# Kernel tuning notes

Measured on AMD Instinct MI355X. Metric: run time of the kernel, lower is better.

## Reference

```python
import jax, jax.numpy as jnp
import numpy as np

B, C, H, W = 64, 1, 1024, 1024
NEG_WEIGHT = 0.1  # constant loss contribution where target != 1


def setup_inputs() -> dict:
    key = jax.random.key(0)
    k1, k2 = jax.random.split(key)
    prediction = jax.random.normal(k1, (B, C, H, W), dtype=jnp.float32)
    target = jax.random.randint(k2, (B, C, H, W), 0, 2, dtype=jnp.int32)
    return {"prediction": prediction, "target": target}


def reference(prediction, target):
    # loss_i = 1 - sigmoid(pred_i) if target_i == 1 else 0.1; return mean over all elements
    p = jax.nn.sigmoid(prediction)
    loss = jnp.where(target == 1, 1.0 - p, jnp.float32(NEG_WEIGHT))
    return jnp.mean(loss)
```

## Files before the change

### kernel.cpp

```cpp
#include <hip/hip_runtime.h>


#define BLOCK 256
#define GRID  2048

typedef float vf4 __attribute__((ext_vector_type(4)));
typedef int   vi4 __attribute__((ext_vector_type(4)));

__device__ __forceinline__ float loss4(vf4 p, vi4 t) {
    float l0 = (t.x == 1) ? 1.0f / (1.0f + __expf(p.x)) : 0.1f;
    float l1 = (t.y == 1) ? 1.0f / (1.0f + __expf(p.y)) : 0.1f;
    float l2 = (t.z == 1) ? 1.0f / (1.0f + __expf(p.z)) : 0.1f;
    float l3 = (t.w == 1) ? 1.0f / (1.0f + __expf(p.w)) : 0.1f;
    return (l0 + l1) + (l2 + l3);
}

__device__ __forceinline__ void block_reduce_atomic(float acc, float inv_n,
                                                    float* __restrict__ out) {
#pragma unroll
    for (int off = 32; off > 0; off >>= 1)
        acc += __shfl_down(acc, off, 64);
    __shared__ float smem[BLOCK / 64];
    const int lane = threadIdx.x & 63;
    const int wave = threadIdx.x >> 6;
    if (lane == 0) smem[wave] = acc;
    __syncthreads();
    if (threadIdx.x == 0) {
        float bsum = (smem[0] + smem[1]) + (smem[2] + smem[3]);
        atomicAdd(out, bsum * inv_n);
    }
}

__global__ __launch_bounds__(BLOCK)
void wloss_nt(const vf4* __restrict__ p4,
              const vi4* __restrict__ t4,
              float* __restrict__ out,
              int iters, int stride, float inv_n) {
    int i = blockIdx.x * BLOCK + threadIdx.x;

    vf4 pA = __builtin_nontemporal_load(&p4[i]);
    vi4 tA = __builtin_nontemporal_load(&t4[i]);
    vf4 pB = __builtin_nontemporal_load(&p4[i + stride]);
    vi4 tB = __builtin_nontemporal_load(&t4[i + stride]);
    int idx = i + 2 * stride;

    float acc = 0.0f;
    for (int k = 0; k < iters - 2; ++k) {
        vf4 pN = __builtin_nontemporal_load(&p4[idx]);
        vi4 tN = __builtin_nontemporal_load(&t4[idx]);
        idx += stride;
        acc += loss4(pA, tA);
        pA = pB; tA = tB;
        pB = pN; tB = tN;
    }
    acc += loss4(pA, tA);
    acc += loss4(pB, tB);

    block_reduce_atomic(acc, inv_n, out);
}

__global__ __launch_bounds__(BLOCK)
void wloss_generic(const float* __restrict__ pred,
                   const int*   __restrict__ tgt,
                   float* __restrict__ out,
                   long long n, float inv_n) {
    const long long n4     = n >> 2;
    const long long tid    = (long long)blockIdx.x * blockDim.x + threadIdx.x;
    const long long stride = (long long)gridDim.x * blockDim.x;

    const vf4* p4 = (const vf4*)pred;
    const vi4* t4 = (const vi4*)tgt;

    float acc = 0.0f;
    for (long long i = tid; i < n4; i += stride)
        acc += loss4(p4[i], t4[i]);
    if (blockIdx.x == 0) {
        for (long long i = (n4 << 2) + threadIdx.x; i < n; i += blockDim.x)
            acc += (tgt[i] == 1) ? 1.0f / (1.0f + __expf(pred[i])) : 0.1f;
    }
    block_reduce_atomic(acc, inv_n, out);
}

extern "C" void kernel_launch(void* const* d_in, const int* in_sizes, int n_in,
                              void* d_out, int out_size, void* d_ws, size_t ws_size,
                              hipStream_t stream) {
    const float* pred = (const float*)d_in[0];
    const int*   tgt  = (const int*)d_in[1];
    float*       out  = (float*)d_out;

    const long long n = (long long)in_sizes[0];
    const float inv_n = 1.0f / (float)n;

    hipMemsetAsync(out, 0, sizeof(float), stream);

    const long long n4 = n >> 2;
    const long long stride = (long long)GRID * BLOCK;

    if ((n & 3) == 0 && n4 % stride == 0 && n4 / stride >= 2) {
        const int iters = (int)(n4 / stride);
        wloss_nt<<<GRID, BLOCK, 0, stream>>>((const vf4*)pred,
                                             (const vi4*)tgt, out,
                                             iters, (int)stride, inv_n);
    } else {
        long long g = (n4 + BLOCK - 1) / BLOCK;
        if (g > 8192) g = 8192;
        if (g < 1)    g = 1;
        wloss_generic<<<(int)g, BLOCK, 0, stream>>>(pred, tgt, out, n, inv_n);
    }
}
```

Baseline: 482.8 us.

## Split into target bitmask pass and prediction pass using workspace

Splits the fused kernel in two. The first kernel packs the target into a 1-bit-per-element ballot mask in workspace and adds the constant 0.1 contributions. The second kernel reads the predictions plus that small mask to sum the sigmoid terms. The total bytes read from global memory stay about the same, plus an extra mask write and read and a second launch, so there is no clear bandwidth saving for this memory-bound reduction.

New measurement: 521.4 us. 8.0% more time.

```diff
diff --git a/kernel.cpp b/kernel.cpp
--- a/kernel.cpp
+++ b/kernel.cpp
@@ -6,6 +6,8 @@
 
 typedef float vf4 __attribute__((ext_vector_type(4)));
 typedef int   vi4 __attribute__((ext_vector_type(4)));
+typedef unsigned long long u64;
+typedef u64 vu2 __attribute__((ext_vector_type(2)));
 
 __device__ __forceinline__ float loss4(vf4 p, vi4 t) {
     float l0 = (t.x == 1) ? 1.0f / (1.0f + __expf(p.x)) : 0.1f;
@@ -15,7 +17,7 @@
     return (l0 + l1) + (l2 + l3);
 }
 
-__device__ __forceinline__ void block_reduce_atomic(float acc, float inv_n,
+__device__ __forceinline__ void block_reduce_atomic(float acc, float scale,
                                                     float* __restrict__ out) {
 #pragma unroll
     for (int off = 32; off > 0; off >>= 1)
@@ -27,8 +29,89 @@
     __syncthreads();
     if (threadIdx.x == 0) {
         float bsum = (smem[0] + smem[1]) + (smem[2] + smem[3]);
-        atomicAdd(out, bsum * inv_n);
-    }
+        atomicAdd(out, bsum * scale);
+    }
+}
+
+__device__ __forceinline__ void tproc(vi4 t, int chunk, int lane,
+                                      u64* __restrict__ mask, int& cnt0) {
+    u64 b0 = __ballot(t.x == 1);
+    u64 b1 = __ballot(t.y == 1);
+    u64 b2 = __ballot(t.z == 1);
+    u64 b3 = __ballot(t.w == 1);
+    cnt0 += (t.x != 1) + (t.y != 1) + (t.z != 1) + (t.w != 1);
+    if (lane < 4) {
+        u64 b = (lane == 0) ? b0 : (lane == 1) ? b1 : (lane == 2) ? b2 : b3;
+        mask[(size_t)chunk * 4 + lane] = b;
+    }
+}
+
+__global__ __launch_bounds__(BLOCK)
+void tgt_mask(const vi4* __restrict__ t4, u64* __restrict__ mask,
+              float* __restrict__ out, int iters, int stride, float inv_n) {
+    const int tid  = threadIdx.x;
+    const int lane = tid & 63;
+    const int wv   = tid >> 6;
+    const int cstep = stride >> 6;
+
+    int i     = blockIdx.x * BLOCK + tid;
+    int chunk = blockIdx.x * (BLOCK / 64) + wv;
+
+    vi4 tA = __builtin_nontemporal_load(&t4[i]);
+    vi4 tB = __builtin_nontemporal_load(&t4[i + stride]);
+    int idx = i + 2 * stride;
+
+    int cnt0 = 0;
+    for (int k = 0; k < iters - 2; ++k) {
+        vi4 tN = __builtin_nontemporal_load(&t4[idx]);
+        idx += stride;
+        tproc(tA, chunk, lane, mask, cnt0);
+        chunk += cstep;
+        tA = tB; tB = tN;
+    }
+    tproc(tA, chunk, lane, mask, cnt0); chunk += cstep;
+    tproc(tB, chunk, lane, mask, cnt0);
+
+    block_reduce_atomic(0.1f * (float)cnt0, inv_n, out);
+}
+
+__device__ __forceinline__ float pproc(vf4 p, const u64* __restrict__ mp, int lane) {
+    vu2 m01 = *(const vu2*)(mp);
+    vu2 m23 = *(const vu2*)(mp + 2);
+    float l0 = ((m01.x >> lane) & 1ull) ? 1.0f / (1.0f + __expf(p.x)) : 0.0f;
+    float l1 = ((m01.y >> lane) & 1ull) ? 1.0f / (1.0f + __expf(p.y)) : 0.0f;
+    float l2 = ((m23.x >> lane) & 1ull) ? 1.0f / (1.0f + __expf(p.z)) : 0.0f;
+    float l3 = ((m23.y >> lane) & 1ull) ? 1.0f / (1.0f + __expf(p.w)) : 0.0f;
+    return (l0 + l1) + (l2 + l3);
+}
+
+__global__ __launch_bounds__(BLOCK)
+void pred_loss(const vf4* __restrict__ p4, const u64* __restrict__ mask,
+               float* __restrict__ out, int iters, int stride, float inv_n) {
+    const int tid  = threadIdx.x;
+    const int lane = tid & 63;
+    const int wv   = tid >> 6;
+    const int cstep = stride >> 6;
+
+    int i     = blockIdx.x * BLOCK + tid;
+    int chunk = blockIdx.x * (BLOCK / 64) + wv;
+
+    vf4 pA = __builtin_nontemporal_load(&p4[i]);
+    vf4 pB = __builtin_nontemporal_load(&p4[i + stride]);
+    int idx = i + 2 * stride;
+
+    float acc = 0.0f;
+    for (int k = 0; k < iters - 2; ++k) {
+        vf4 pN = __builtin_nontemporal_load(&p4[idx]);
+        idx += stride;
+        acc += pproc(pA, mask + (size_t)chunk * 4, lane);
+        chunk += cstep;
+        pA = pB; pB = pN;
+    }
+    acc += pproc(pA, mask + (size_t)chunk * 4, lane); chunk += cstep;
+    acc += pproc(pB, mask + (size_t)chunk * 4, lane);
+
+    block_reduce_atomic(acc, inv_n, out);
 }
 
 __global__ __launch_bounds__(BLOCK)
@@ -95,8 +178,17 @@
 
     const long long n4 = n >> 2;
     const long long stride = (long long)GRID * BLOCK;
-
-    if ((n & 3) == 0 && n4 % stride == 0 && n4 / stride >= 2) {
+    const bool tiled = ((n & 3) == 0) && (n4 % stride == 0) && (n4 / stride >= 3);
+    const size_t mask_bytes = (size_t)(n >> 3);
+
+    if (tiled && d_ws != nullptr && ws_size >= mask_bytes) {
+        const int iters = (int)(n4 / stride);
+        u64* mask = (u64*)d_ws;
+        tgt_mask <<<GRID, BLOCK, 0, stream>>>((const vi4*)tgt, mask, out,
+                                              iters, (int)stride, inv_n);
+        pred_loss<<<GRID, BLOCK, 0, stream>>>((const vf4*)pred, mask, out,
+                                              iters, (int)stride, inv_n);
+    } else if (tiled) {
         const int iters = (int)(n4 / stride);
         wloss_nt<<<GRID, BLOCK, 0, stream>>>((const vf4*)pred,
                                              (const vi4*)tgt, out,
```

## Stream inputs through LDS with global_load_lds double buffering

Applied to the files above, without the earlier changes.

The main streaming kernel now fetches prediction and target tiles with direct global-to-LDS loads into a two-slot shared buffer, reads them back from LDS and syncs the block each iteration. Register-held prefetch is dropped so more loads can be in flight without using VGPRs. In exchange it adds a block barrier per iteration and an extra LDS read. It also loses the nontemporal hint, and the 16-byte global_load_lds width may not be supported on every target.

After: 507.0 us. 5.0% more time.

```diff
diff --git a/kernel.cpp b/kernel.cpp
--- a/kernel.cpp
+++ b/kernel.cpp
@@ -7,6 +7,9 @@
 typedef float vf4 __attribute__((ext_vector_type(4)));
 typedef int   vi4 __attribute__((ext_vector_type(4)));
 
+typedef const __attribute__((address_space(1))) void glb_v;
+typedef __attribute__((address_space(3))) void lds_v;
+
 __device__ __forceinline__ float loss4(vf4 p, vi4 t) {
     float l0 = (t.x == 1) ? 1.0f / (1.0f + __expf(p.x)) : 0.1f;
     float l1 = (t.y == 1) ? 1.0f / (1.0f + __expf(p.y)) : 0.1f;
@@ -15,7 +18,7 @@
     return (l0 + l1) + (l2 + l3);
 }
 
-__device__ __forceinline__ void block_reduce_atomic(float acc, float inv_n,
+__device__ __forceinline__ void block_reduce_atomic(float acc, float scale,
                                                     float* __restrict__ out) {
 #pragma unroll
     for (int off = 32; off > 0; off >>= 1)
@@ -27,34 +30,41 @@
     __syncthreads();
     if (threadIdx.x == 0) {
         float bsum = (smem[0] + smem[1]) + (smem[2] + smem[3]);
-        atomicAdd(out, bsum * inv_n);
+        atomicAdd(out, bsum * scale);
     }
 }
 
 __global__ __launch_bounds__(BLOCK)
-void wloss_nt(const vf4* __restrict__ p4,
-              const vi4* __restrict__ t4,
-              float* __restrict__ out,
-              int iters, int stride, float inv_n) {
-    int i = blockIdx.x * BLOCK + threadIdx.x;
+void wl_main_dma(const vf4* __restrict__ p4,
+                 const vi4* __restrict__ t4,
+                 float* __restrict__ out,
+                 int iters, int stride, float inv_n) {
+    __shared__ vf4 lp[2][BLOCK];
+    __shared__ vi4 lt[2][BLOCK];
 
-    vf4 pA = __builtin_nontemporal_load(&p4[i]);
-    vi4 tA = __builtin_nontemporal_load(&t4[i]);
-    vf4 pB = __builtin_nontemporal_load(&p4[i + stride]);
-    vi4 tB = __builtin_nontemporal_load(&t4[i + stride]);
-    int idx = i + 2 * stride;
+    const int tid = threadIdx.x;
+    const int wv  = tid >> 6;
+    int idx = blockIdx.x * BLOCK + tid;
+
+    __builtin_amdgcn_global_load_lds((glb_v*)&p4[idx], (lds_v*)&lp[0][wv * 64], 16, 0, 0);
+    __builtin_amdgcn_global_load_lds((glb_v*)&t4[idx], (lds_v*)&lt[0][wv * 64], 16, 0, 0);
+    __syncthreads();
 
     float acc = 0.0f;
-    for (int k = 0; k < iters - 2; ++k) {
-        vf4 pN = __builtin_nontemporal_load(&p4[idx]);
-        vi4 tN = __builtin_nontemporal_load(&t4[idx]);
+    int cur = 0;
+    for (int k = 0; k < iters - 1; ++k) {
         idx += stride;
-        acc += loss4(pA, tA);
-        pA = pB; tA = tB;
-        pB = pN; tB = tN;
+        __builtin_amdgcn_global_load_lds((glb_v*)&p4[idx], (lds_v*)&lp[cur ^ 1][wv * 64], 16, 0, 0);
+        __builtin_amdgcn_global_load_lds((glb_v*)&t4[idx], (lds_v*)&lt[cur ^ 1][wv * 64], 16, 0, 0);
+        vf4 p = lp[cur][tid];
+        vi4 t = lt[cur][tid];
+        acc += loss4(p, t);
+        __syncthreads();
+        cur ^= 1;
     }
-    acc += loss4(pA, tA);
-    acc += loss4(pB, tB);
+    vf4 p = lp[cur][tid];
+    vi4 t = lt[cur][tid];
+    acc += loss4(p, t);
 
     block_reduce_atomic(acc, inv_n, out);
 }
@@ -95,12 +105,13 @@
 
     const long long n4 = n >> 2;
     const long long stride = (long long)GRID * BLOCK;
+    const bool tiled = ((n & 3) == 0) && (n4 % stride == 0) && (n4 / stride >= 2);
 
-    if ((n & 3) == 0 && n4 % stride == 0 && n4 / stride >= 2) {
+    if (tiled) {
         const int iters = (int)(n4 / stride);
-        wloss_nt<<<GRID, BLOCK, 0, stream>>>((const vf4*)pred,
-                                             (const vi4*)tgt, out,
-                                             iters, (int)stride, inv_n);
+        wl_main_dma<<<GRID, BLOCK, 0, stream>>>((const vf4*)pred,
+                                                (const vi4*)tgt, out,
+                                                iters, (int)stride, inv_n);
     } else {
         long long g = (n4 + BLOCK - 1) / BLOCK;
         if (g > 8192) g = 8192;
```
